# Optimization experiments

Hardware: AMD Instinct MI355X
Metric: run time of the kernel (lower is better)

## Reference

```python
import jax, jax.numpy as jnp
import numpy as np
from jax import lax

B, T, E, H, V, D_ACT, OUT = 128, 512, 12, 512, 16, 10, 64


def setup_inputs() -> dict:
    key = jax.random.key(0)
    ks = jax.random.split(key, 9)
    ts = jax.random.uniform(ks[0], (B, T, 2), dtype=jnp.float32)
    idx = jax.random.randint(ks[1], (B, T), 0, V).astype(jnp.float32)
    x = jnp.concatenate([ts, idx[..., None]], axis=-1)  # [B,T,3], col2 = activity ids
    emb = jax.random.normal(ks[2], (V, D_ACT), jnp.float32) * 0.1
    emb = emb.at[0].set(0.0)  # padding_idx=0
    W_fwd = jax.random.normal(ks[3], (E, 3 * H), jnp.float32) / np.sqrt(E).astype(np.float32)
    b_fwd = jnp.zeros((3 * H,), jnp.float32)
    W_bwd = jax.random.normal(ks[4], (E, 3 * H), jnp.float32) / np.sqrt(E).astype(np.float32)
    b_bwd = jnp.zeros((3 * H,), jnp.float32)
    weight_Mu = jax.random.normal(ks[5], (2 * H, 1), jnp.float32) * 0.1
    W_out = jax.random.normal(ks[6], (OUT, 2 * H), jnp.float32) * 0.01  # torch Linear layout [out,in]
    b_out = jnp.zeros((OUT,), jnp.float32)
    return {"x": x, "emb": emb, "W_fwd": W_fwd, "b_fwd": b_fwd,
            "W_bwd": W_bwd, "b_bwd": b_bwd, "weight_Mu": weight_Mu,
            "W_out": W_out, "b_out": b_out}


def _fo_pool(z, f):
    # h_t = f_t * h_{t-1} + (1 - f_t) * z_t, scanned over time (axis 0)
    def step(c, zf):
        z_t, f_t = zf
        c = f_t * c + (1.0 - f_t) * z_t
        return c, c
    c0 = jnp.zeros_like(z[0])
    _, cs = lax.scan(step, c0, (z, f))
    return cs  # [T,B,H]


def _qrnn_dir(inp, W, b):
    # inp: [T,B,E] -> gates [T,B,3H]
    Y = inp @ W + b
    Z, F_, O = jnp.split(Y, 3, axis=-1)
    Z = jnp.tanh(Z)
    F_ = jax.nn.sigmoid(F_)
    O = jax.nn.sigmoid(O)
    C = _fo_pool(Z, F_)
    return O * C  # [T,B,H]


def reference(x, emb, W_fwd, b_fwd, W_bwd, b_bwd, weight_Mu, W_out, b_out):
    ts = x[:, :, :2]                                   # [B,T,2] time features
    act = emb[x[:, :, 2].astype(jnp.int32)]            # [B,T,10]
    enc = jnp.concatenate([ts, act], axis=-1)          # [B,T,E]
    inp = jnp.transpose(enc, (1, 0, 2))                # [T,B,E]
    h_f = _qrnn_dir(inp, W_fwd, b_fwd)                 # [T,B,H]
    h_b = _qrnn_dir(inp[::-1], W_bwd, b_bwd)[::-1]     # reverse-direction QRNN
    out = jnp.concatenate([h_f, h_b], axis=-1)         # [T,B,2H]
    out = jax.nn.relu(jnp.transpose(out, (1, 0, 2)))   # [B,T,2H]
    attn = jax.nn.softmax(out @ weight_Mu, axis=1)     # [B,T,1], softmax over time
    context = jnp.einsum('btd,bt->bd', out, attn[..., 0])  # [B,2H]
    context = jax.nn.relu(context)
    return context @ W_out.T + b_out                   # [B,OUT]
```

## Files before the change

kernel.cpp:

```cpp
#include <hip/hip_runtime.h>
#include <hip/hip_bf16.h>

#define B_   128
#define T_   512
#define H_   512
#define V_   16
#define OUT_ 64
#define DH_  1024
#define NCH  8


#define TAB_BYTES (V_*H_*16)
#define TSA_BYTES (T_*8)
#define VPK_BYTES (T_)
#define SCAN_LDS  (TAB_BYTES + TSA_BYTES + VPK_BYTES)

#define LOG2E 1.4426950408889634f

__device__ __forceinline__ float bf2f_lo(unsigned int u) {
    union { unsigned int i; float f; } x; x.i = u << 16; return x.f;
}
__device__ __forceinline__ float bf2f_hi(unsigned int u) {
    union { unsigned int i; float f; } x; x.i = u & 0xffff0000u; return x.f;
}

__global__ __launch_bounds__(512) void qrnn_scan9(
    const float* __restrict__ x,
    const float* __restrict__ emb,
    const float* __restrict__ Wf, const float* __restrict__ bf_,
    const float* __restrict__ Wb, const float* __restrict__ bb_,
    __hip_bfloat16* __restrict__ hbuf)
{
    const int b = blockIdx.x, dir = blockIdx.y, h = threadIdx.x;
    const float* __restrict__ W    = dir ? Wb  : Wf;
    const float* __restrict__ bias = dir ? bb_ : bf_;

    extern __shared__ char smem[];
    float4*        tab = (float4*)smem;
    float2*        tsA = (float2*)(smem + TAB_BYTES);
    unsigned char* vpk = (unsigned char*)(smem + TAB_BYTES + TSA_BYTES);

    {
        const int t = h;
        const float* xp = x + ((size_t)b*T_ + t)*3;
        tsA[t] = make_float2(xp[0], xp[1]);
        vpk[t] = (unsigned char)(int)xp[2];
    }

    float w0[3], w1[3], wt[10][3];
#pragma unroll
    for (int g = 0; g < 3; ++g) {
        w0[g] = W[g*H_ + h];
        w1[g] = W[1536 + g*H_ + h];
#pragma unroll
        for (int e = 0; e < 10; ++e)
            wt[e][g] = W[(2+e)*1536 + g*H_ + h];
    }
    const float bz = bias[h], bfv = bias[H_+h], bov = bias[2*H_+h];

    const float FZ = -2.8853900817779268f;
    const float FF = -1.4426950408889634f;

#pragma unroll
    for (int v = 0; v < V_; ++v) {
        float a0 = bz, a1 = bfv, a2 = bov;
#pragma unroll
        for (int e = 0; e < 10; ++e) {
            const float ev = emb[v*10 + e];
            a0 = fmaf(ev, wt[e][0], a0);
            a1 = fmaf(ev, wt[e][1], a1);
            a2 = fmaf(ev, wt[e][2], a2);
        }
        tab[v*H_ + h] = make_float4(FZ*a0, FF*a1, FF*a2, 0.f);
    }
    const float w0z = FZ*w0[0], w0f = FF*w0[1], w0o = FF*w0[2];
    const float w1z = FZ*w1[0], w1f = FF*w1[1], w1o = FF*w1[2];
    __syncthreads();

    const float4* tsA4 = (const float4*)tsA;
    const uint2*  vp2  = (const uint2*)vpk;

    float c = 0.f;
    __hip_bfloat16* hb = hbuf + (size_t)b*DH_ + dir*H_ + h;

#define SS(i, A0, A1, G) { \
    const float zp = fmaf(A0, w0z, fmaf(A1, w1z, (G).x)); \
    const float fp = fmaf(A0, w0f, fmaf(A1, w1f, (G).y)); \
    const float op = fmaf(A0, w0o, fmaf(A1, w1o, (G).z)); \
    const float rz = __builtin_amdgcn_rcpf(1.f + __builtin_amdgcn_exp2f(zp)); \
    const float f  = __builtin_amdgcn_rcpf(1.f + __builtin_amdgcn_exp2f(fp)); \
    const float o  = __builtin_amdgcn_rcpf(1.f + __builtin_amdgcn_exp2f(op)); \
    const float z  = fmaf(2.f, rz, -1.f); \
    c = fmaf(f, c - z, z); \
    const float hv = fmaxf(o * c, 0.f); \
    hb[(size_t)(t0 + (i))*(B_*DH_)] = __float2bfloat16(hv); \
}

#pragma unroll 2
    for (int gi = 0; gi < T_/8; ++gi) {
        const int gg = dir ? (T_/8 - 1 - gi) : gi;
        const int t0 = gg*8;
        const uint2  vp  = vp2[gg];
        const float4 tsa = tsA4[gg*4 + 0];
        const float4 tsb = tsA4[gg*4 + 1];
        const float4 tsc = tsA4[gg*4 + 2];
        const float4 tsd = tsA4[gg*4 + 3];
        const int v0 =  vp.x        & 255, v1 = (vp.x >> 8) & 255;
        const int v2 = (vp.x >> 16) & 255, v3 =  vp.x >> 24;
        const int v4 =  vp.y        & 255, v5 = (vp.y >> 8) & 255;
        const int v6 = (vp.y >> 16) & 255, v7 =  vp.y >> 24;
        const float4 g0 = tab[v0*H_ + h];
        const float4 g1 = tab[v1*H_ + h];
        const float4 g2 = tab[v2*H_ + h];
        const float4 g3 = tab[v3*H_ + h];
        const float4 g4 = tab[v4*H_ + h];
        const float4 g5 = tab[v5*H_ + h];
        const float4 g6 = tab[v6*H_ + h];
        const float4 g7 = tab[v7*H_ + h];
        if (dir == 0) {
            SS(0, tsa.x, tsa.y, g0) SS(1, tsa.z, tsa.w, g1)
            SS(2, tsb.x, tsb.y, g2) SS(3, tsb.z, tsb.w, g3)
            SS(4, tsc.x, tsc.y, g4) SS(5, tsc.z, tsc.w, g5)
            SS(6, tsd.x, tsd.y, g6) SS(7, tsd.z, tsd.w, g7)
        } else {
            SS(7, tsd.z, tsd.w, g7) SS(6, tsd.x, tsd.y, g6)
            SS(5, tsc.z, tsc.w, g5) SS(4, tsc.x, tsc.y, g4)
            SS(3, tsb.z, tsb.w, g3) SS(2, tsb.x, tsb.y, g2)
            SS(1, tsa.z, tsa.w, g1) SS(0, tsa.x, tsa.y, g0)
        }
    }
#undef SS
}

__global__ __launch_bounds__(512) void postfuse2(
    const __hip_bfloat16* __restrict__ hbuf,
    const float* __restrict__ Mu,
    float* __restrict__ pctx,
    float* __restrict__ pesum)
{
    const int b    = blockIdx.x;
    const int q    = blockIdx.y;
    const int w    = threadIdx.x >> 6;
    const int lane = threadIdx.x & 63;

    __shared__ float pw[8][DH_];
    __shared__ float psum[8];

    float mu[16];
    const float4* mp = (const float4*)Mu;
#pragma unroll
    for (int k = 0; k < 2; ++k) {
        const float4 m0 = mp[(k*64 + lane)*2];
        const float4 m1 = mp[(k*64 + lane)*2 + 1];
        mu[k*8+0]=m0.x; mu[k*8+1]=m0.y; mu[k*8+2]=m0.z; mu[k*8+3]=m0.w;
        mu[k*8+4]=m1.x; mu[k*8+5]=m1.y; mu[k*8+6]=m1.z; mu[k*8+7]=m1.w;
    }

    float acc[16];
#pragma unroll
    for (int i = 0; i < 16; ++i) acc[i] = 0.f;
    float esum = 0.f;

#pragma unroll 2
    for (int j = 0; j < 8; ++j) {
        const int t = q*64 + j*8 + w;
        const uint4* hp = (const uint4*)(hbuf + ((size_t)t*B_ + b)*DH_);
        const uint4 u0 = hp[lane];
        const uint4 u1 = hp[64 + lane];
        float hv[16];
        hv[0]  = bf2f_lo(u0.x); hv[1]  = bf2f_hi(u0.x);
        hv[2]  = bf2f_lo(u0.y); hv[3]  = bf2f_hi(u0.y);
        hv[4]  = bf2f_lo(u0.z); hv[5]  = bf2f_hi(u0.z);
        hv[6]  = bf2f_lo(u0.w); hv[7]  = bf2f_hi(u0.w);
        hv[8]  = bf2f_lo(u1.x); hv[9]  = bf2f_hi(u1.x);
        hv[10] = bf2f_lo(u1.y); hv[11] = bf2f_hi(u1.y);
        hv[12] = bf2f_lo(u1.z); hv[13] = bf2f_hi(u1.z);
        hv[14] = bf2f_lo(u1.w); hv[15] = bf2f_hi(u1.w);

        float s = 0.f;
#pragma unroll
        for (int i = 0; i < 16; ++i) s = fmaf(hv[i], mu[i], s);
#pragma unroll
        for (int off = 1; off <= 32; off <<= 1) s += __shfl_xor(s, off);

        const float e = __builtin_amdgcn_exp2f(s * LOG2E);
        esum += e;
#pragma unroll
        for (int i = 0; i < 16; ++i) acc[i] = fmaf(hv[i], e, acc[i]);
    }

#pragma unroll
    for (int k = 0; k < 2; ++k) {
        *(float4*)&pw[w][k*512 + lane*8]     = make_float4(acc[k*8+0], acc[k*8+1], acc[k*8+2], acc[k*8+3]);
        *(float4*)&pw[w][k*512 + lane*8 + 4] = make_float4(acc[k*8+4], acc[k*8+5], acc[k*8+6], acc[k*8+7]);
    }
    if (lane == 0) psum[w] = esum;
    __syncthreads();

    {
        const int d = threadIdx.x;
        float c0 = 0.f, c1 = 0.f;
#pragma unroll
        for (int i = 0; i < 8; ++i) { c0 += pw[i][d]; c1 += pw[i][d + 512]; }
        float* pc = pctx + ((size_t)b*NCH + q)*DH_;
        pc[d]       = c0;
        pc[d + 512] = c1;
    }
    if (threadIdx.x == 0) {
        float ts = 0.f;
#pragma unroll
        for (int i = 0; i < 8; ++i) ts += psum[i];
        pesum[b*NCH + q] = ts;
    }
}

__global__ __launch_bounds__(512) void combine_out(
    const float* __restrict__ pctx,
    const float* __restrict__ pesum,
    const float* __restrict__ Wout,
    const float* __restrict__ bout,
    float* __restrict__ out)
{
    const int b    = blockIdx.x;
    const int w    = threadIdx.x >> 6;
    const int lane = threadIdx.x & 63;

    __shared__ float ctx[DH_];
    __shared__ float rinv_s;

    {
        const int d = threadIdx.x;
        const float* pc = pctx + (size_t)b*NCH*DH_;
        float c0 = 0.f, c1 = 0.f;
#pragma unroll
        for (int i = 0; i < NCH; ++i) { c0 += pc[i*DH_ + d]; c1 += pc[i*DH_ + d + 512]; }
        ctx[d]       = fmaxf(c0, 0.f);
        ctx[d + 512] = fmaxf(c1, 0.f);
    }
    if (threadIdx.x == 0) {
        float ts = 0.f;
#pragma unroll
        for (int i = 0; i < NCH; ++i) ts += pesum[b*NCH + i];
        rinv_s = __builtin_amdgcn_rcpf(ts);
    }
    __syncthreads();

    const float rinv = rinv_s;
#pragma unroll
    for (int oo = 0; oo < 8; ++oo) {
        const int o = w*8 + oo;
        const float* wp = Wout + o*DH_;
        float a = 0.f;
#pragma unroll
        for (int k = 0; k < 16; ++k) {
            const int d = k*64 + lane;
            a = fmaf(ctx[d], wp[d], a);
        }
#pragma unroll
        for (int off = 1; off <= 32; off <<= 1) a += __shfl_xor(a, off);
        if (lane == 0) out[b*OUT_ + o] = a*rinv + bout[o];
    }
}

extern "C" void kernel_launch(void* const* d_in, const int* in_sizes, int n_in,
                              void* d_out, int out_size, void* d_ws, size_t ws_size,
                              hipStream_t stream)
{
    const float* x    = (const float*)d_in[0];
    const float* emb  = (const float*)d_in[1];
    const float* Wf   = (const float*)d_in[2];
    const float* bf_  = (const float*)d_in[3];
    const float* Wb   = (const float*)d_in[4];
    const float* bb_  = (const float*)d_in[5];
    const float* Mu   = (const float*)d_in[6];
    const float* Wout = (const float*)d_in[7];
    const float* bout = (const float*)d_in[8];
    float* out = (float*)d_out;

    char* ws = (char*)d_ws;
    const size_t hbytes = (size_t)B_*T_*DH_*sizeof(__hip_bfloat16);
    __hip_bfloat16* hbuf = (__hip_bfloat16*)ws;
    float* pctx  = (float*)(ws + hbytes);
    float* pesum = pctx + (size_t)B_*NCH*DH_;

    (void)hipFuncSetAttribute((const void*)qrnn_scan9,
                              hipFuncAttributeMaxDynamicSharedMemorySize,
                              SCAN_LDS);

    qrnn_scan9<<<dim3(B_, 2), 512, SCAN_LDS, stream>>>(x, emb, Wf, bf_, Wb, bb_, hbuf);
    postfuse2<<<dim3(B_, NCH), 512, 0, stream>>>(hbuf, Mu, pctx, pesum);
    combine_out<<<B_, 512, 0, stream>>>(pctx, pesum, Wout, bout, out);
}
```

Measured before the change: 170.3 us.

## Store hidden states batch-major and rework attention pooling into 32-step chunks

The scan kernel now writes hidden states in [B,T,2H] layout instead of [T,B,2H]. Each thread writes with a stride of one row instead of a whole batch plane, and the pooling kernel reads contiguous memory per batch. The pooling kernel is rewritten to use 256 threads per block over 16 time chunks of 32 steps. Each wave handles a quarter of the feature dimension, and the partial dot products are combined through LDS with extra barriers. The intent is more coalesced, more local stores in the scan and more blocks in the pooling pass, at the cost of more synchronisation and more partial results for the combine kernel to sum.

```diff
diff --git a/kernel.cpp b/kernel.cpp
--- a/kernel.cpp
+++ b/kernel.cpp
@@ -7,7 +7,7 @@
 #define V_   16
 #define OUT_ 64
 #define DH_  1024
-#define NCH  8
+#define NCH  16
 
 
 #define TAB_BYTES (V_*H_*16)
@@ -24,7 +24,7 @@
     union { unsigned int i; float f; } x; x.i = u & 0xffff0000u; return x.f;
 }
 
-__global__ __launch_bounds__(512) void qrnn_scan9(
+__global__ __launch_bounds__(512) void qrnn_scan12(
     const float* __restrict__ x,
     const float* __restrict__ emb,
     const float* __restrict__ Wf, const float* __restrict__ bf_,
@@ -81,7 +81,7 @@
     const uint2*  vp2  = (const uint2*)vpk;
 
     float c = 0.f;
-    __hip_bfloat16* hb = hbuf + (size_t)b*DH_ + dir*H_ + h;
+    __hip_bfloat16* hb = hbuf + (size_t)b*T_*DH_ + dir*H_ + h;
 
 #define SS(i, A0, A1, G) { \
     const float zp = fmaf(A0, w0z, fmaf(A1, w1z, (G).x)); \
@@ -93,7 +93,7 @@
     const float z  = fmaf(2.f, rz, -1.f); \
     c = fmaf(f, c - z, z); \
     const float hv = fmaxf(o * c, 0.f); \
-    hb[(size_t)(t0 + (i))*(B_*DH_)] = __float2bfloat16(hv); \
+    hb[(size_t)(t0 + (i))*DH_] = __float2bfloat16(hv); \
 }
 
 #pragma unroll 2
@@ -132,85 +132,81 @@
 #undef SS
 }
 
-__global__ __launch_bounds__(512) void postfuse2(
+__global__ __launch_bounds__(256) void postfuse10(
     const __hip_bfloat16* __restrict__ hbuf,
     const float* __restrict__ Mu,
     float* __restrict__ pctx,
     float* __restrict__ pesum)
 {
-    const int b    = blockIdx.x;
-    const int q    = blockIdx.y;
+    const int q    = blockIdx.x;
+    const int b    = blockIdx.y;
     const int w    = threadIdx.x >> 6;
     const int lane = threadIdx.x & 63;
-
-    __shared__ float pw[8][DH_];
-    __shared__ float psum[8];
-
-    float mu[16];
-    const float4* mp = (const float4*)Mu;
-#pragma unroll
-    for (int k = 0; k < 2; ++k) {
-        const float4 m0 = mp[(k*64 + lane)*2];
-        const float4 m1 = mp[(k*64 + lane)*2 + 1];
-        mu[k*8+0]=m0.x; mu[k*8+1]=m0.y; mu[k*8+2]=m0.z; mu[k*8+3]=m0.w;
-        mu[k*8+4]=m1.x; mu[k*8+5]=m1.y; mu[k*8+6]=m1.z; mu[k*8+7]=m1.w;
-    }
-
-    float acc[16];
-#pragma unroll
-    for (int i = 0; i < 16; ++i) acc[i] = 0.f;
-    float esum = 0.f;
-
-#pragma unroll 2
-    for (int j = 0; j < 8; ++j) {
-        const int t = q*64 + j*8 + w;
-        const uint4* hp = (const uint4*)(hbuf + ((size_t)t*B_ + b)*DH_);
-        const uint4 u0 = hp[lane];
-        const uint4 u1 = hp[64 + lane];
-        float hv[16];
-        hv[0]  = bf2f_lo(u0.x); hv[1]  = bf2f_hi(u0.x);
-        hv[2]  = bf2f_lo(u0.y); hv[3]  = bf2f_hi(u0.y);
-        hv[4]  = bf2f_lo(u0.z); hv[5]  = bf2f_hi(u0.z);
-        hv[6]  = bf2f_lo(u0.w); hv[7]  = bf2f_hi(u0.w);
-        hv[8]  = bf2f_lo(u1.x); hv[9]  = bf2f_hi(u1.x);
-        hv[10] = bf2f_lo(u1.y); hv[11] = bf2f_hi(u1.y);
-        hv[12] = bf2f_lo(u1.z); hv[13] = bf2f_hi(u1.z);
-        hv[14] = bf2f_lo(u1.w); hv[15] = bf2f_hi(u1.w);
-
-        float s = 0.f;
-#pragma unroll
-        for (int i = 0; i < 16; ++i) s = fmaf(hv[i], mu[i], s);
-#pragma unroll
-        for (int off = 1; off <= 32; off <<= 1) s += __shfl_xor(s, off);
-
-        const float e = __builtin_amdgcn_exp2f(s * LOG2E);
-        esum += e;
-#pragma unroll
-        for (int i = 0; i < 16; ++i) acc[i] = fmaf(hv[i], e, acc[i]);
-    }
-
-#pragma unroll
-    for (int k = 0; k < 2; ++k) {
-        *(float4*)&pw[w][k*512 + lane*8]     = make_float4(acc[k*8+0], acc[k*8+1], acc[k*8+2], acc[k*8+3]);
-        *(float4*)&pw[w][k*512 + lane*8 + 4] = make_float4(acc[k*8+4], acc[k*8+5], acc[k*8+6], acc[k*8+7]);
-    }
-    if (lane == 0) psum[w] = esum;
-    __syncthreads();
-
-    {
-        const int d = threadIdx.x;
-        float c0 = 0.f, c1 = 0.f;
-#pragma unroll
-        for (int i = 0; i < 8; ++i) { c0 += pw[i][d]; c1 += pw[i][d + 512]; }
-        float* pc = pctx + ((size_t)b*NCH + q)*DH_;
-        pc[d]       = c0;
-        pc[d + 512] = c1;
-    }
-    if (threadIdx.x == 0) {
-        float ts = 0.f;
-#pragma unroll
-        for (int i = 0; i < 8; ++i) ts += psum[i];
-        pesum[b*NCH + q] = ts;
+    const int t0   = q*32;
+
+    __shared__ float ps[4][8];
+    __shared__ float e_lds[8];
+
+    const float4 mu = ((const float4*)(Mu + w*256))[lane];
+
+    const char* base = (const char*)hbuf + ((size_t)b*T_ + t0)*(DH_*2)
+                       + w*512 + lane*8;
+
+    float a0 = 0.f, a1 = 0.f, a2 = 0.f, a3 = 0.f;
+    float es_priv = 0.f;
+
+#pragma unroll
+    for (int g = 0; g < 4; ++g) {
+        uint2 U0, U1, U2, U3, U4, U5, U6, U7;
+        U0 = *(const uint2*)(base + (g*8+0)*2048);
+        U1 = *(const uint2*)(base + (g*8+1)*2048);
+        U2 = *(const uint2*)(base + (g*8+2)*2048);
+        U3 = *(const uint2*)(base + (g*8+3)*2048);
+        U4 = *(const uint2*)(base + (g*8+4)*2048);
+        U5 = *(const uint2*)(base + (g*8+5)*2048);
+        U6 = *(const uint2*)(base + (g*8+6)*2048);
+        U7 = *(const uint2*)(base + (g*8+7)*2048);
+
+#define DOTROW(j, U) { \
+        float s = fmaf(bf2f_lo(U.x), mu.x, fmaf(bf2f_hi(U.x), mu.y, \
+                  fmaf(bf2f_lo(U.y), mu.z, bf2f_hi(U.y) * mu.w))); \
+        s += __shfl_xor(s, 1);  s += __shfl_xor(s, 2); \
+        s += __shfl_xor(s, 4);  s += __shfl_xor(s, 8); \
+        s += __shfl_xor(s, 16); s += __shfl_xor(s, 32); \
+        if (lane == 0) ps[w][j] = s; }
+        DOTROW(0, U0) DOTROW(1, U1) DOTROW(2, U2) DOTROW(3, U3)
+        DOTROW(4, U4) DOTROW(5, U5) DOTROW(6, U6) DOTROW(7, U7)
+#undef DOTROW
+        __syncthreads();
+
+        if (threadIdx.x < 8) {
+            const int j = threadIdx.x;
+            const float sj = ps[0][j] + ps[1][j] + ps[2][j] + ps[3][j];
+            const float ej = __builtin_amdgcn_exp2f(sj * LOG2E);
+            es_priv += ej;
+            e_lds[j] = ej;
+        }
+        __syncthreads();
+
+#define ACCROW(j, U) { \
+        const float ej = e_lds[j]; \
+        a0 = fmaf(bf2f_lo(U.x), ej, a0); \
+        a1 = fmaf(bf2f_hi(U.x), ej, a1); \
+        a2 = fmaf(bf2f_lo(U.y), ej, a2); \
+        a3 = fmaf(bf2f_hi(U.y), ej, a3); }
+        ACCROW(0, U0) ACCROW(1, U1) ACCROW(2, U2) ACCROW(3, U3)
+        ACCROW(4, U4) ACCROW(5, U5) ACCROW(6, U6) ACCROW(7, U7)
+#undef ACCROW
+        __syncthreads();
+    }
+
+    float4* pc = (float4*)(pctx + ((size_t)b*NCH + q)*DH_ + w*256);
+    pc[lane] = make_float4(a0, a1, a2, a3);
+
+    if (w == 0) {
+        float t = es_priv;
+        t += __shfl_xor(t, 1); t += __shfl_xor(t, 2); t += __shfl_xor(t, 4);
+        if (lane == 0) pesum[b*NCH + q] = t;
     }
 }
 
@@ -283,11 +279,11 @@
     float* pctx  = (float*)(ws + hbytes);
     float* pesum = pctx + (size_t)B_*NCH*DH_;
 
-    (void)hipFuncSetAttribute((const void*)qrnn_scan9,
+    (void)hipFuncSetAttribute((const void*)qrnn_scan12,
                               hipFuncAttributeMaxDynamicSharedMemorySize,
                               SCAN_LDS);
 
-    qrnn_scan9<<<dim3(B_, 2), 512, SCAN_LDS, stream>>>(x, emb, Wf, bf_, Wb, bb_, hbuf);
-    postfuse2<<<dim3(B_, NCH), 512, 0, stream>>>(hbuf, Mu, pctx, pesum);
+    qrnn_scan12<<<dim3(B_, 2), 512, SCAN_LDS, stream>>>(x, emb, Wf, bf_, Wb, bb_, hbuf);
+    postfuse10<<<dim3(NCH, B_), 256, 0, stream>>>(hbuf, Mu, pctx, pesum);
     combine_out<<<B_, 512, 0, stream>>>(pctx, pesum, Wout, bout, out);
 }
```

Measured after the change: 171.4 us. No clear change (+0.7%).
